# Kernel optimization log

Hardware: AMD Instinct MI355X
Metric: run time of the kernel (lower is better)

Reference implementation:

```python
import jax, jax.numpy as jnp
import numpy as np
import math

B, T = 32, 64
VOCAB = 50005
EMB = 512
HID = 1024
SES = 1024
KNOW = 8785
NEG = math.exp(-100)

def _glorot(key, shape):
    fan_in, fan_out = shape[1], shape[0]
    lim = (6.0 / (fan_in + fan_out)) ** 0.5
    return jax.random.uniform(key, shape, jnp.float32, -lim, lim)

def setup_inputs() -> dict:
    key = jax.random.key(0)
    ks = jax.random.split(key, 16)
    inp = {}
    inp['ses_encoding'] = jax.random.normal(ks[0], (B, 1, SES), jnp.float32)
    inp['know_encoding'] = jax.random.normal(ks[1], (B, 1, SES), jnp.float32)
    inp['target'] = jax.random.randint(ks[2], (B, T), 0, 50000)
    inp['embed_w'] = jax.random.normal(ks[3], (VOCAB, EMB), jnp.float32) * 0.02
    # GRU params (PyTorch layout: W_ih [3H, E], W_hh [3H, H], gate order r,z,n)
    s = 1.0 / (HID ** 0.5)
    inp['W_ih'] = jax.random.uniform(ks[4], (3 * HID, EMB), jnp.float32, -s, s)
    inp['W_hh'] = jax.random.uniform(ks[5], (3 * HID, HID), jnp.float32, -s, s)
    inp['b_ih'] = jax.random.uniform(ks[6], (3 * HID,), jnp.float32, -s, s)
    inp['b_hh'] = jax.random.uniform(ks[7], (3 * HID,), jnp.float32, -s, s)
    inp['ses_to_dec_w'] = _glorot(ks[8], (HID, SES))
    inp['ses_to_dec_b'] = jnp.zeros((HID,), jnp.float32)
    inp['dec_inf_w'] = _glorot(ks[9], (2 * EMB, HID))
    inp['ses_inf_w'] = _glorot(ks[10], (2 * EMB, SES))
    inp['emb_inf_w'] = _glorot(ks[11], (2 * EMB, EMB))
    inp['emb_inf_b'] = jnp.zeros((2 * EMB,), jnp.float32)
    inp['W1'] = jax.random.normal(ks[12], (VOCAB, SES), jnp.float32) * 0.02
    inp['W2'] = jax.random.normal(ks[13], (VOCAB, SES), jnp.float32) * 0.02
    inp['W3'] = jax.random.normal(ks[14], (VOCAB, 2 * EMB), jnp.float32) * 0.02
    inp['W4'] = jax.random.normal(ks[15], (VOCAB, EMB), jnp.float32) * 0.02
    inp['know_vote_w'] = _glorot(jax.random.fold_in(key, 99), (KNOW, SES))
    return inp

def _gru_step(x, h, W_ih, W_hh, b_ih, b_hh):
    # x: [B,E], h: [B,H]
    gi = x @ W_ih.T + b_ih
    gh = h @ W_hh.T + b_hh
    ir, iz, inn = jnp.split(gi, 3, axis=-1)
    hr, hz, hn = jnp.split(gh, 3, axis=-1)
    r = jax.nn.sigmoid(ir + hr)
    z = jax.nn.sigmoid(iz + hz)
    n = jnp.tanh(inn + r * hn)
    return (1.0 - z) * h + z * n  # torch: h' = (1-z)*n + z*h with torch z; note torch formula

def _gru_step_torch(x, h, W_ih, W_hh, b_ih, b_hh):
    gi = x @ W_ih.T + b_ih
    gh = h @ W_hh.T + b_hh
    ir, iz, inn = jnp.split(gi, 3, axis=-1)
    hr, hz, hn = jnp.split(gh, 3, axis=-1)
    r = jax.nn.sigmoid(ir + hr)
    z = jax.nn.sigmoid(iz + hz)
    n = jnp.tanh(inn + r * hn)
    return (1.0 - z) * n + z * h

def reference(ses_encoding, know_encoding, target, embed_w, W_ih, W_hh, b_ih, b_hh,
              ses_to_dec_w, ses_to_dec_b, dec_inf_w, ses_inf_w, emb_inf_w, emb_inf_b,
              W1, W2, W3, W4, know_vote_w):
    ses = ses_encoding[:, 0, :]    # [B, SES]
    know = know_encoding[:, 0, :]  # [B, SES]
    target_emb = embed_w[target]   # [B, T, E]

    h0 = jnp.tanh(ses @ ses_to_dec_w.T + ses_to_dec_b)  # [B, H]

    # time-invariant pieces
    ses_inf_vec = ses @ ses_inf_w.T                      # [B, 2E]
    l1 = ses @ W1.T                                      # [B, V]
    l2 = know @ W2.T                                     # [B, V]
    # knowledge mixture log-probs (constant over time)
    ks = know @ know_vote_w.T                            # [B, KNOW]
    ks = ks[:, :-1]                                      # drop last -> [B, KNOW-1]
    pad_l = jnp.full((ks.shape[0], 10), NEG, ks.dtype)
    pad_r = jnp.full((ks.shape[0], VOCAB - 10 - (KNOW - 1)), NEG, ks.dtype)
    know_scores = jnp.concatenate([pad_l, ks, pad_r], axis=1)  # [B, V]
    know_probs = jax.nn.log_softmax(know_scores, axis=-1)      # [B, V]
    gate_const = l1 + l2                                 # [B, V]

    def step(h, emb_t):
        # emb_t: [B, E]
        h_new = _gru_step_torch(emb_t, h, W_ih, W_hh, b_ih, b_hh)  # [B, H]
        dec_hid_vec = h_new @ dec_inf_w.T                          # [B, 2E]
        target_inf = emb_t @ emb_inf_w.T + emb_inf_b               # [B, 2E]
        total = dec_hid_vec + ses_inf_vec + target_inf             # [B, 2E]
        mx = jnp.max(total.reshape(total.shape[0], EMB, 2), axis=-1)  # maxout -> [B, E]
        logits = mx @ embed_w.T                                    # shared embedding -> [B, V]
        hid_probs = jax.nn.log_softmax(logits, axis=-1)
        l3 = h_new @ W3.T                                          # note: W3 applied to hid_o [B,H]... but W3 is [V,2E]
        l4 = emb_t @ W4.T                                          # [B, V]
        gate = jax.nn.sigmoid(gate_const + l3 + l4)                # [B, V]
        final = gate * hid_probs + (1.0 - gate) * know_probs       # [B, V]
        return h_new, final

    # target_emb time-major for scan
    _, outs = jax.lax.scan(step, h0, jnp.swapaxes(target_emb, 0, 1))
    final_scores_all = jnp.swapaxes(outs, 0, 1)  # [B, T, V]
    return final_scores_all
```

## Files before the change

kernel.cpp:

```cpp
#include <hip/hip_runtime.h>

constexpr int VOC  = 50005;
constexpr int VOCP = 50048;
constexpr int VOCP2= 50176;
constexpr int NTM  = 391;
constexpr int NTMP = 400;
constexpr int KSN  = 8784;
constexpr float NPAD = 41221.0f;

typedef unsigned short u16;
typedef __attribute__((ext_vector_type(4))) float f32x4;
typedef __attribute__((ext_vector_type(8))) short bf16x8;

__device__ __forceinline__ float dot4(float4 a, float4 b) {
    return a.x*b.x + a.y*b.y + a.z*b.z + a.w*b.w;
}
__device__ __forceinline__ float sigmoidf_(float x) { return 1.0f / (1.0f + expf(-x)); }
__device__ __forceinline__ u16 f2bf(float f) {
    unsigned x = __float_as_uint(f);
    return (u16)((x + 0x7FFFu + ((x >> 16) & 1u)) >> 16);
}
__device__ __forceinline__ float bf2f(u16 u) { return __uint_as_float(((unsigned)u) << 16); }
__device__ __forceinline__ bf16x8 pack8(float4 lo, float4 hi) {
    union { bf16x8 v; unsigned u[4]; } r;
    r.u[0] = f2bf(lo.x) | ((unsigned)f2bf(lo.y) << 16);
    r.u[1] = f2bf(lo.z) | ((unsigned)f2bf(lo.w) << 16);
    r.u[2] = f2bf(hi.x) | ((unsigned)f2bf(hi.y) << 16);
    r.u[3] = f2bf(hi.z) | ((unsigned)f2bf(hi.w) << 16);
    return r.v;
}
template<int AUX>
__device__ __forceinline__ void gload_lds16x(const void* g, void* l) {
    __builtin_amdgcn_global_load_lds((const __attribute__((address_space(1))) unsigned int*)g,
                                     (__attribute__((address_space(3))) unsigned int*)l, 16, 0, AUX);
}
__device__ __forceinline__ void gload_lds16(const void* g, void* l) { gload_lds16x<0>(g, l); }
__device__ __forceinline__ void store_u16_sc(u16* p, u16 v) {
    asm volatile("global_store_short %0, %1, off sc0 sc1" :: "v"(p), "v"((unsigned)v) : "memory");
}

__global__ __launch_bounds__(256) void k_cvt(const float* __restrict__ src, u16* __restrict__ dst,
                                             int ncols, int sld, int dld) {
    int row = blockIdx.x;
    int c = (blockIdx.y * 256 + threadIdx.x) * 4;
    if (c >= ncols) return;
    float4 v = *(const float4*)(src + (size_t)row * sld + c);
    unsigned lo = f2bf(v.x) | ((unsigned)f2bf(v.y) << 16);
    unsigned hi = f2bf(v.z) | ((unsigned)f2bf(v.w) << 16);
    *(uint2*)(dst + (size_t)row * dld + c) = make_uint2(lo, hi);
}

__global__ __launch_bounds__(256) void k_pad0(u16* __restrict__ Aemb, u16* __restrict__ A34) {
    int r = VOC + blockIdx.x;
    unsigned* p3 = (unsigned*)(A34 + (size_t)r * 1536);
    for (int i = threadIdx.x; i < 768; i += 256) p3[i] = 0;
    if (r < VOCP) {
        unsigned* pe = (unsigned*)(Aemb + (size_t)r * 512);
        if (threadIdx.x < 256) pe[threadIdx.x] = 0;
    }
}

__global__ __launch_bounds__(256) void k_bsk(const float* __restrict__ ses,
                                             const float* __restrict__ know,
                                             u16* __restrict__ Bsk) {
    int row = blockIdx.x;
    for (int c0 = threadIdx.x * 4; c0 < 2048; c0 += 1024) {
        uint2 val = make_uint2(0, 0);
        if (row < 32) {
            const float* srcp = (c0 < 1024) ? ses + (size_t)row * 1024 + c0
                                            : know + (size_t)row * 1024 + (c0 - 1024);
            float4 v = *(const float4*)srcp;
            val = make_uint2(f2bf(v.x) | ((unsigned)f2bf(v.y) << 16),
                             f2bf(v.z) | ((unsigned)f2bf(v.w) << 16));
        }
        *(uint2*)(Bsk + (size_t)row * 2048 + c0) = val;
    }
}

__global__ __launch_bounds__(128) void k_gather(const float* __restrict__ embed,
                                                const int* __restrict__ target,
                                                u16* __restrict__ BG) {
    int n = blockIdx.x;
    int row = target[n];
    int c = threadIdx.x * 4;
    float4 v = *(const float4*)(embed + (size_t)row * 512 + c);
    unsigned lo = f2bf(v.x) | ((unsigned)f2bf(v.y) << 16);
    unsigned hi = f2bf(v.z) | ((unsigned)f2bf(v.w) << 16);
    *(uint2*)(BG + (size_t)n * 1536 + 1024 + c) = make_uint2(lo, hi);
}

__global__ __launch_bounds__(256) void k_h0_sesinf(const float* __restrict__ ses,
                                                   const float* __restrict__ sdw,
                                                   const float* __restrict__ sdb,
                                                   const float* __restrict__ siw,
                                                   float* __restrict__ h0,
                                                   float* __restrict__ sesinf) {
    int g = blockIdx.x * 256 + threadIdx.x;
    int b = g & 31;
    int jg = g >> 5;
    int j0 = jg * 4;
    const float4* s4 = (const float4*)(ses + (size_t)b * 1024);
    const float4* wa[4];
    const float4* wc[4];
#pragma unroll
    for (int r = 0; r < 4; ++r) {
        wa[r] = (const float4*)(sdw + (size_t)(j0 + r) * 1024);
        wc[r] = (const float4*)(siw + (size_t)(j0 + r) * 1024);
    }
    float a[4] = {0, 0, 0, 0}, c[4] = {0, 0, 0, 0};
    for (int kq = 0; kq < 256; ++kq) {
        float4 sv = s4[kq];
#pragma unroll
        for (int r = 0; r < 4; ++r) { a[r] += dot4(sv, wa[r][kq]); c[r] += dot4(sv, wc[r][kq]); }
    }
#pragma unroll
    for (int r = 0; r < 4; ++r) {
        h0[b * 1024 + j0 + r] = tanhf(a[r] + sdb[j0 + r]);
        sesinf[b * 1024 + j0 + r] = c[r];
    }
}

__global__ __launch_bounds__(256) void k_lseknow(const float* __restrict__ ks,
                                                 float* __restrict__ lsek) {
    int b = blockIdx.x;
    int t = threadIdx.x;
    __shared__ float sm[256];
    float m = -1e30f;
    for (int j = t; j < KSN; j += 256) m = fmaxf(m, ks[(size_t)b * KSN + j]);
    sm[t] = m;
    __syncthreads();
    for (int s = 128; s > 0; s >>= 1) { if (t < s) sm[t] = fmaxf(sm[t], sm[t + s]); __syncthreads(); }
    m = fmaxf(sm[0], 0.0f);
    __syncthreads();
    float s = 0.0f;
    for (int j = t; j < KSN; j += 256) s += expf(ks[(size_t)b * KSN + j] - m);
    sm[t] = s;
    __syncthreads();
    for (int r = 128; r > 0; r >>= 1) { if (t < r) sm[t] += sm[t + r]; __syncthreads(); }
    if (t == 0) lsek[b] = m + logf(sm[0] + NPAD * expf(0.0f - m));
}

template<int MODE>
__global__ __launch_bounds__(128) void k_sk32(const float* __restrict__ A1,
                                              const float* __restrict__ A2,
                                              const u16* __restrict__ Bsk,
                                              float* __restrict__ outp) {
    const int lane = threadIdx.x & 63;
    const int w = threadIdx.x >> 6;
    const int lrow = lane & 15;
    const int kg = lane >> 4;
    constexpr int K = (MODE == 0) ? 2048 : 1024;
    constexpr int bc0 = (MODE == 0) ? 0 : 1024;
    const int rowmax = (MODE == 0) ? (VOC - 1) : (KSN - 1);
    const int vb = blockIdx.x * 64 + w * 32;
    const int r0 = min(vb + lrow, rowmax);
    const int r1 = min(vb + 16 + lrow, rowmax);
    f32x4 acc[2][2] = {{{0.f,0.f,0.f,0.f},{0.f,0.f,0.f,0.f}},
                       {{0.f,0.f,0.f,0.f},{0.f,0.f,0.f,0.f}}};
    for (int k0 = 0; k0 < K; k0 += 32) {
        int kc = k0 + kg * 8;
        const float* s0;
        const float* s1;
        if (MODE == 0 && k0 >= 1024) {
            s0 = A2 + (size_t)r0 * 1024 + (kc - 1024);
            s1 = A2 + (size_t)r1 * 1024 + (kc - 1024);
        } else {
            s0 = A1 + (size_t)r0 * 1024 + kc;
            s1 = A1 + (size_t)r1 * 1024 + kc;
        }
        bf16x8 af0 = pack8(*(const float4*)s0, *(const float4*)(s0 + 4));
        bf16x8 af1 = pack8(*(const float4*)s1, *(const float4*)(s1 + 4));
        bf16x8 b0 = *(const bf16x8*)(Bsk + (size_t)lrow * 2048 + bc0 + kc);
        bf16x8 b1 = *(const bf16x8*)(Bsk + (size_t)(16 + lrow) * 2048 + bc0 + kc);
        acc[0][0] = __builtin_amdgcn_mfma_f32_16x16x32_bf16(af0, b0, acc[0][0], 0, 0, 0);
        acc[0][1] = __builtin_amdgcn_mfma_f32_16x16x32_bf16(af0, b1, acc[0][1], 0, 0, 0);
        acc[1][0] = __builtin_amdgcn_mfma_f32_16x16x32_bf16(af1, b0, acc[1][0], 0, 0, 0);
        acc[1][1] = __builtin_amdgcn_mfma_f32_16x16x32_bf16(af1, b1, acc[1][1], 0, 0, 0);
    }
    const int rg = kg * 4;
#pragma unroll
    for (int mi = 0; mi < 2; ++mi)
#pragma unroll
        for (int ni = 0; ni < 2; ++ni)
#pragma unroll
            for (int r = 0; r < 4; ++r) {
                int v = vb + mi * 16 + rg + r;
                int b = ni * 16 + lrow;
                if (MODE == 0) outp[(size_t)b * VOCP2 + v] = acc[mi][ni][r];
                else if (v < KSN) outp[(size_t)b * KSN + v] = acc[mi][ni][r];
            }
}

template<int EPI>
__global__ __launch_bounds__(256) void gemm_bt(
    const u16* __restrict__ A, int lda,
    const u16* __restrict__ B, int ldb, int K,
    const float* __restrict__ p0, const float* __restrict__ p1,
    float* __restrict__ q0, u16* __restrict__ q1,
    unsigned char* __restrict__ q2, float* __restrict__ q3)
{
    __shared__ u16 Asm[128 * 64];
    __shared__ u16 Bsm[128 * 64];
    const int tid = threadIdx.x;
    const int lane = tid & 63;
    const int w = tid >> 6;
    const int wm = w >> 1, wn = w & 1;
    const int nt = blockIdx.x, mt = blockIdx.y;

    f32x4 acc[4][4];
#pragma unroll
    for (int i = 0; i < 4; ++i)
#pragma unroll
        for (int j = 0; j < 4; ++j) acc[i][j] = (f32x4){0.f, 0.f, 0.f, 0.f};

    for (int kt = 0; kt < K; kt += 64) {
#pragma unroll
        for (int p = 0; p < 4; ++p) {
            int flat = (w * 4 + p) * 64 + lane;
            int row = flat >> 3, slot = flat & 7;
            int ss = slot ^ (row & 7);
            gload_lds16(A + (size_t)(mt * 128 + row) * lda + kt + ss * 8, Asm + flat * 8);
            gload_lds16(B + (size_t)(nt * 128 + row) * ldb + kt + ss * 8, Bsm + flat * 8);
        }
        __syncthreads();
#pragma unroll
        for (int kc = 0; kc < 2; ++kc) {
            bf16x8 af[4], bfr[4];
#pragma unroll
            for (int mi = 0; mi < 4; ++mi) {
                int row = wm * 64 + mi * 16 + (lane & 15);
                int bcol = kc * 64 + ((lane >> 4) << 4);
                af[mi] = *(const bf16x8*)((const char*)Asm + row * 128 + (bcol ^ ((row & 7) << 4)));
            }
#pragma unroll
            for (int ni = 0; ni < 4; ++ni) {
                int row = wn * 64 + ni * 16 + (lane & 15);
                int bcol = kc * 64 + ((lane >> 4) << 4);
                bfr[ni] = *(const bf16x8*)((const char*)Bsm + row * 128 + (bcol ^ ((row & 7) << 4)));
            }
#pragma unroll
            for (int mi = 0; mi < 4; ++mi)
#pragma unroll
                for (int ni = 0; ni < 4; ++ni)
                    acc[mi][ni] = __builtin_amdgcn_mfma_f32_16x16x32_bf16(af[mi], bfr[ni], acc[mi][ni], 0, 0, 0);
        }
        __syncthreads();
    }

    const int cl = lane & 15;
    const int rg = (lane >> 4) << 2;

    if constexpr (EPI == 0) {
#pragma unroll
        for (int mi = 0; mi < 4; ++mi) {
            int m0 = mt * 128 + wm * 64 + mi * 16 + rg;
            float4 bias = *(const float4*)(p0 + m0);
#pragma unroll
            for (int ni = 0; ni < 4; ++ni) {
                int n = nt * 128 + wn * 64 + ni * 16 + cl;
                float4 v;
                v.x = acc[mi][ni][0] + bias.x; v.y = acc[mi][ni][1] + bias.y;
                v.z = acc[mi][ni][2] + bias.z; v.w = acc[mi][ni][3] + bias.w;
                *(float4*)(q0 + (size_t)n * 3072 + m0) = v;
            }
        }
    }
    if constexpr (EPI == 1) {
#pragma unroll
        for (int mi = 0; mi < 4; ++mi) {
            int m0 = mt * 128 + wm * 64 + mi * 16 + rg;
            float4 eb4 = *(const float4*)(p1 + m0);
#pragma unroll
            for (int ni = 0; ni < 4; ++ni) {
                int n = nt * 128 + wn * 64 + ni * 16 + cl;
                int b = n >> 6;
                float v0 = acc[mi][ni][0] + p0[b * 1024 + m0 + 0] + eb4.x;
                float v1 = acc[mi][ni][1] + p0[b * 1024 + m0 + 1] + eb4.y;
                float v2 = acc[mi][ni][2] + p0[b * 1024 + m0 + 2] + eb4.z;
                float v3 = acc[mi][ni][3] + p0[b * 1024 + m0 + 3] + eb4.w;
                unsigned pk = f2bf(fmaxf(v0, v1)) | ((unsigned)f2bf(fmaxf(v2, v3)) << 16);
                *(unsigned*)(q1 + (size_t)n * 512 + (m0 >> 1)) = pk;
            }
        }
    }
    if constexpr (EPI == 3) {
        __shared__ float redm[2][128];
        __shared__ float reds[2][128];
#pragma unroll
        for (int mi = 0; mi < 4; ++mi) {
            int v0 = mt * 128 + wm * 64 + mi * 16 + rg;
#pragma unroll
            for (int ni = 0; ni < 4; ++ni) {
                int n = nt * 128 + wn * 64 + ni * 16 + cl;
                unsigned lo = f2bf(acc[mi][ni][0]) | ((unsigned)f2bf(acc[mi][ni][1]) << 16);
                unsigned hi = f2bf(acc[mi][ni][2]) | ((unsigned)f2bf(acc[mi][ni][3]) << 16);
                *(uint2*)(q1 + (size_t)n * VOCP + v0) = make_uint2(lo, hi);
            }
        }
#pragma unroll
        for (int ni = 0; ni < 4; ++ni) {
            float lm = -1e30f;
#pragma unroll
            for (int mi = 0; mi < 4; ++mi) {
                int v0 = mt * 128 + wm * 64 + mi * 16 + rg;
#pragma unroll
                for (int r = 0; r < 4; ++r)
                    if (v0 + r < VOC) lm = fmaxf(lm, acc[mi][ni][r]);
            }
            lm = fmaxf(lm, __shfl_xor(lm, 16));
            lm = fmaxf(lm, __shfl_xor(lm, 32));
            float s = 0.0f;
#pragma unroll
            for (int mi = 0; mi < 4; ++mi) {
                int v0 = mt * 128 + wm * 64 + mi * 16 + rg;
#pragma unroll
                for (int r = 0; r < 4; ++r)
                    if (v0 + r < VOC) s += expf(acc[mi][ni][r] - lm);
            }
            s += __shfl_xor(s, 16);
            s += __shfl_xor(s, 32);
            if (lane < 16) {
                redm[wm][wn * 64 + ni * 16 + lane] = lm;
                reds[wm][wn * 64 + ni * 16 + lane] = s;
            }
        }
        __syncthreads();
        if (tid < 128) {
            float m0_ = redm[0][tid], m1_ = redm[1][tid];
            float m = fmaxf(m0_, m1_);
            float s = reds[0][tid] * expf(m0_ - m) + reds[1][tid] * expf(m1_ - m);
            int n = nt * 128 + tid;
            q0[(size_t)n * NTMP + mt] = m;
            q3[(size_t)n * NTMP + mt] = s;
        }
    }
}

__global__ __launch_bounds__(512, 1) void gemm_gate8(
    const u16* __restrict__ A,
    const u16* __restrict__ B,
    const float* __restrict__ gc2,
    unsigned char* __restrict__ g8)
{
    __shared__ __align__(16) char smem[131072];
    const int tid = threadIdx.x;
    const int lane = tid & 63;
    const int w = tid >> 6;
    const int wm = w >> 2;
    const int wn = w & 3;
    const int lrow = lane & 15;
    const int g = lane >> 4;

    int bid = blockIdx.x;
    int wg = (bid & 7) * 196 + (bid >> 3);
    int mt = wg >> 3;
    int nt = wg & 7;
    const size_t arow0 = (size_t)mt * 256;
    const size_t brow0 = (size_t)nt * 256;

    auto stageA = [&](int T, int h) {
        char* dst = smem + (T & 1) * 65536 + h * 16384;
        const u16* src = A + (arow0 + h * 128) * 1536 + T * 64;
#pragma unroll
        for (int q = 0; q < 2; ++q) {
            int flat = q * 512 + tid;
            int r = flat >> 3, s = flat & 7;
            int ss = s ^ (r & 7);
            gload_lds16(src + (size_t)r * 1536 + ss * 8, dst + flat * 16);
        }
    };
    auto stageB = [&](int T, int h) {
        char* dst = smem + (T & 1) * 65536 + 32768 + h * 16384;
        const u16* src = B + (brow0 + h * 128) * 1536 + T * 64;
#pragma unroll
        for (int q = 0; q < 2; ++q) {
            int flat = q * 512 + tid;
            int r = flat >> 3, s = flat & 7;
            int ss = s ^ (r & 7);
            gload_lds16(src + (size_t)r * 1536 + ss * 8, dst + flat * 16);
        }
    };

    f32x4 acc[8][4];
#pragma unroll
    for (int i = 0; i < 8; ++i)
#pragma unroll
        for (int j = 0; j < 4; ++j) acc[i][j] = (f32x4){0.f, 0.f, 0.f, 0.f};

    const char* Ab[2] = { smem + wm * 16384, smem + 65536 + wm * 16384 };
    const char* Bb[2] = { smem + 32768 + (wn >> 1) * 16384,
                          smem + 65536 + 32768 + (wn >> 1) * 16384 };
    bf16x8 bf[4][2];
    bf16x8 afA[2][2], afB[2][2];

#define ISSA(D, Q, AF)                                                                \
    _Pragma("unroll") for (int mi = 0; mi < 2; ++mi) {                                \
        int r = ((Q) * 2 + mi) * 16 + lrow;                                           \
        _Pragma("unroll") for (int kk = 0; kk < 2; ++kk)                              \
            AF[mi][kk] = *(const bf16x8*)(Ab[D] + r * 128 +                           \
                            ((kk * 64 + g * 16) ^ ((r & 7) << 4)));                   \
    }
#define ISSB(D)                                                                       \
    _Pragma("unroll") for (int ni = 0; ni < 4; ++ni) {                                \
        int r = (wn & 1) * 64 + ni * 16 + lrow;                                       \
        _Pragma("unroll") for (int kk = 0; kk < 2; ++kk)                              \
            bf[ni][kk] = *(const bf16x8*)(Bb[D] + r * 128 +                           \
                            ((kk * 64 + g * 16) ^ ((r & 7) << 4)));                   \
    }
#define MM(Q, AF)                                                                     \
    __builtin_amdgcn_s_setprio(1);                                                    \
    _Pragma("unroll") for (int kk = 0; kk < 2; ++kk)                                  \
        _Pragma("unroll") for (int mi = 0; mi < 2; ++mi)                              \
            _Pragma("unroll") for (int ni = 0; ni < 4; ++ni)                          \
                acc[(Q) * 2 + mi][ni] = __builtin_amdgcn_mfma_f32_16x16x32_bf16(      \
                    AF[mi][kk], bf[ni][kk], acc[(Q) * 2 + mi][ni], 0, 0, 0);          \
    __builtin_amdgcn_s_setprio(0)
#define LG4 asm volatile("s_waitcnt lgkmcnt(4)" ::: "memory"); __builtin_amdgcn_sched_barrier(0)
#define LG0 asm volatile("s_waitcnt lgkmcnt(0)" ::: "memory"); __builtin_amdgcn_sched_barrier(0)
#define BARR  __builtin_amdgcn_sched_barrier(0); __builtin_amdgcn_s_barrier(); \
              __builtin_amdgcn_sched_barrier(0)
#define VM4 asm volatile("s_waitcnt vmcnt(4)" ::: "memory"); __builtin_amdgcn_sched_barrier(0)
#define VM0 asm volatile("s_waitcnt vmcnt(0)" ::: "memory"); __builtin_amdgcn_sched_barrier(0)

    stageB(0, 0); stageB(0, 1); stageA(0, 0); stageA(0, 1); stageB(1, 0); stageB(1, 1);
    VM4;
    BARR;
    ISSA(0, 0, afA);

    for (int i = 0; i < 11; ++i) {
        int T0 = 2 * i, T1 = 2 * i + 1;
        stageA(T1, 0); ISSB(0); ISSA(0, 1, afB); LG4; MM(0, afA);
        stageA(T1, 1); ISSA(0, 2, afA); LG4; MM(1, afB);
        BARR;
        stageB(T0 + 2, 0); ISSA(0, 3, afB); LG4; MM(2, afA);
        stageB(T0 + 2, 1); VM4; ISSA(1, 0, afA); LG4; MM(3, afB);
        BARR;
        stageA(T0 + 2, 0); ISSB(1); ISSA(1, 1, afB); LG4; MM(0, afA);
        stageA(T0 + 2, 1); ISSA(1, 2, afA); LG4; MM(1, afB);
        BARR;
        stageB(T1 + 2, 0); ISSA(1, 3, afB); LG4; MM(2, afA);
        stageB(T1 + 2, 1); VM4; ISSA(0, 0, afA); LG4; MM(3, afB);
        BARR;
    }
    stageA(23, 0); ISSB(0); ISSA(0, 1, afB); LG4; MM(0, afA);
    stageA(23, 1); ISSA(0, 2, afA); LG4; MM(1, afB);
    BARR;
    ISSA(0, 3, afB); LG4; MM(2, afA);
    VM0; ISSA(1, 0, afA); LG4; MM(3, afB);
    BARR;
    ISSB(1); ISSA(1, 1, afB); LG4; MM(0, afA);
    ISSA(1, 2, afA); LG4; MM(1, afB);
    ISSA(1, 3, afB); LG4; MM(2, afA);
    LG0; MM(3, afB);
#undef ISSA
#undef ISSB
#undef MM
#undef LG4
#undef LG0
#undef BARR
#undef VM4
#undef VM0

    const int rg = g << 2;
    const int b = nt * 4 + wn;
    const float* gcrow = gc2 + (size_t)b * VOCP2;
#pragma unroll
    for (int m = 0; m < 8; ++m) {
        int v0 = mt * 256 + wm * 128 + m * 16 + rg;
        float4 gcv = *(const float4*)(gcrow + v0);
#pragma unroll
        for (int ni = 0; ni < 4; ++ni) {
            int n = nt * 256 + wn * 64 + ni * 16 + lrow;
            unsigned pk = 0;
#pragma unroll
            for (int r = 0; r < 4; ++r) {
                float garg = acc[m][ni][r] + ((const float*)&gcv)[r];
                float gate = 1.0f / (1.0f + expf(-garg));
                pk |= ((unsigned)(int)(gate * 255.0f + 0.5f)) << (8 * r);
            }
            *(unsigned*)(g8 + (size_t)n * VOCP2 + v0) = pk;
        }
    }
}

__global__ __launch_bounds__(256, 1) void k_gru_m4(const u16* __restrict__ WhhB,
                                                   const float* __restrict__ GI,
                                                   const float* __restrict__ bhh,
                                                   const u16* __restrict__ h0b,
                                                   u16* __restrict__ BG,
                                                   unsigned* __restrict__ flags) {
    __shared__ __align__(16) char smem[131072];
    const int tid = threadIdx.x;
    const int lane = tid & 63;
    const int w = tid >> 6;
    const int jb = blockIdx.x;
    const int j0 = jb * 16;
    const int jl = tid & 15, bp = tid >> 4;
    const int je = j0 + jl;
    const float bh0 = bhh[je], bh1 = bhh[1024 + je], bh2 = bhh[2048 + je];
    char* Bbase = smem + 98304 + w * 8192;

#pragma unroll
    for (int it = 0; it < 24; ++it) {
        int flat = (it * 4 + w) * 64 + lane;
        int r = flat >> 7, s = flat & 127;
        int ss = s ^ (r & 7);
        int gr = (r >> 4) * 1024 + j0 + (r & 15);
        gload_lds16(WhhB + (size_t)gr * 1024 + ss * 8, smem + (size_t)flat * 16);
    }

    float hpv[2];
#pragma unroll
    for (int rb = 0; rb < 2; ++rb)
        hpv[rb] = bf2f(h0b[(size_t)(bp * 2 + rb) * 1024 + je]);

    const int lrow = lane & 15;
    const int ksel = lane >> 4;

    for (int t = 0; t < 64; ++t) {
        const u16* hsrc = (t == 0) ? h0b : BG + (size_t)(t - 1) * 1536;
        const size_t hstr = (t == 0) ? 1024 : (size_t)64 * 1536;

        float gi0[2], gi1[2], gi2[2];
#pragma unroll
        for (int rb = 0; rb < 2; ++rb) {
            const float* gp = GI + ((size_t)((bp * 2 + rb) * 64 + t)) * 3072 + je;
            gi0[rb] = gp[0]; gi1[rb] = gp[1024]; gi2[rb] = gp[2048];
        }
        __builtin_amdgcn_sched_barrier(0);

        auto stageB = [&](int c) {
            char* dst = Bbase + (c & 1) * 4096;
            int kq0 = w * 256 + c * 64;
#pragma unroll
            for (int q = 0; q < 4; ++q) {
                int flat = q * 64 + lane;
                int r = flat >> 3, s = flat & 7;
                int ss = s ^ (r & 7);
                gload_lds16x<0x11>(hsrc + (size_t)r * hstr + kq0 + ss * 8,
                                   dst + (size_t)flat * 16);
            }
        };
        stageB(0); stageB(1);
        if (t == 0) {
            __syncthreads();
        } else {
            asm volatile("s_waitcnt vmcnt(4)" ::: "memory");
        }
        __builtin_amdgcn_sched_barrier(0);

        f32x4 acc[3][2];
#pragma unroll
        for (int mi = 0; mi < 3; ++mi)
#pragma unroll
            for (int ni = 0; ni < 2; ++ni) acc[mi][ni] = (f32x4){0.f, 0.f, 0.f, 0.f};

#pragma unroll
        for (int c = 0; c < 4; ++c) {
            char* Bb = Bbase + (c & 1) * 4096;
#pragma unroll
            for (int ks = 0; ks < 2; ++ks) {
                int kb = ks * 64 + ksel * 16;
                bf16x8 bfr[2];
#pragma unroll
                for (int ni = 0; ni < 2; ++ni) {
                    int br = ni * 16 + lrow;
                    bfr[ni] = *(const bf16x8*)(Bb + br * 128 + (kb ^ ((br & 7) << 4)));
                }
                int kA = w * 512 + c * 128 + kb;
#pragma unroll
                for (int mi = 0; mi < 3; ++mi) {
                    int ar = mi * 16 + lrow;
                    bf16x8 af = *(const bf16x8*)(smem + ar * 2048 + (kA ^ ((ar & 7) << 4)));
#pragma unroll
                    for (int ni = 0; ni < 2; ++ni)
                        acc[mi][ni] = __builtin_amdgcn_mfma_f32_16x16x32_bf16(af, bfr[ni], acc[mi][ni], 0, 0, 0);
                }
            }
            asm volatile("s_waitcnt lgkmcnt(0)" ::: "memory");
            __builtin_amdgcn_sched_barrier(0);
            if (c < 2) {
                stageB(c + 2);
                asm volatile("s_waitcnt vmcnt(4)" ::: "memory");
            } else if (c == 2) {
                asm volatile("s_waitcnt vmcnt(0)" ::: "memory");
            }
            __builtin_amdgcn_sched_barrier(0);
        }

        float (*epiw)[33] = (float(*)[33])Bbase;
        {
            const int rg = (lane >> 4) << 2;
#pragma unroll
            for (int mi = 0; mi < 3; ++mi)
#pragma unroll
                for (int ni = 0; ni < 2; ++ni) {
                    int m0 = mi * 16 + rg;
                    int cb = ni * 16 + lrow;
#pragma unroll
                    for (int r = 0; r < 4; ++r) epiw[m0 + r][cb] = acc[mi][ni][r];
                }
        }
        asm volatile("s_waitcnt lgkmcnt(0)" ::: "memory");
        __builtin_amdgcn_s_barrier();

#pragma unroll
        for (int rb = 0; rb < 2; ++rb) {
            int b = bp * 2 + rb;
            float s0 = 0.f, s1 = 0.f, s2 = 0.f;
#pragma unroll
            for (int ww = 0; ww < 4; ++ww) {
                float (*ep)[33] = (float(*)[33])(smem + 98304 + ww * 8192);
                s0 += ep[jl][b]; s1 += ep[16 + jl][b]; s2 += ep[32 + jl][b];
            }
            float rr = sigmoidf_(gi0[rb] + s0 + bh0);
            float zz = sigmoidf_(gi1[rb] + s1 + bh1);
            float nn = tanhf(gi2[rb] + rr * (s2 + bh2));
            float hnew = (1.0f - zz) * nn + zz * hpv[rb];
            hpv[rb] = hnew;
            store_u16_sc(BG + ((size_t)(b * 64 + t)) * 1536 + je, f2bf(hnew));
        }

        if (t < 63) {
            asm volatile("s_waitcnt vmcnt(0)" ::: "memory");
            __syncthreads();
            if (tid == 0)
                __hip_atomic_store(&flags[jb], (unsigned)(t + 1),
                                   __ATOMIC_RELAXED, __HIP_MEMORY_SCOPE_AGENT);
            unsigned tgt = (unsigned)(t + 1);
            while (true) {
                unsigned v = __hip_atomic_load(&flags[lane],
                                               __ATOMIC_RELAXED, __HIP_MEMORY_SCOPE_AGENT);
                if (__all(v >= tgt)) break;
                __builtin_amdgcn_s_sleep(1);
            }
            __builtin_amdgcn_sched_barrier(0);
        }
    }
}

__global__ __launch_bounds__(256) void k_lse(const float* __restrict__ pmax,
                                             const float* __restrict__ psum,
                                             float* __restrict__ lse) {
    int n = blockIdx.x;
    int t = threadIdx.x;
    __shared__ float sm[256];
    const float* pm = pmax + (size_t)n * NTMP;
    const float* ps = psum + (size_t)n * NTMP;
    float m = -1e30f;
    for (int p = t; p < NTM; p += 256) m = fmaxf(m, pm[p]);
    sm[t] = m;
    __syncthreads();
    for (int s = 128; s > 0; s >>= 1) { if (t < s) sm[t] = fmaxf(sm[t], sm[t + s]); __syncthreads(); }
    m = sm[0];
    __syncthreads();
    float s = 0.0f;
    for (int p = t; p < NTM; p += 256) s += ps[p] * expf(pm[p] - m);
    sm[t] = s;
    __syncthreads();
    for (int r = 128; r > 0; r >>= 1) { if (t < r) sm[t] += sm[t + r]; __syncthreads(); }
    if (t == 0) lse[n] = m + logf(sm[0]);
}

__global__ __launch_bounds__(256) void k_final(const u16* __restrict__ Lb,
                                               const unsigned char* __restrict__ g8,
                                               const float* __restrict__ lse,
                                               const float* __restrict__ ks,
                                               const float* __restrict__ lsek,
                                               float* __restrict__ out) {
    int n = blockIdx.y;
    int b = n >> 6;
    float lsen = lse[n], lkb = lsek[b];
    int base = blockIdx.x * 2048;
#pragma unroll
    for (int i = 0; i < 8; ++i) {
        int v = base + i * 256 + threadIdx.x;
        if (v < VOC) {
            float L = bf2f(Lb[(size_t)n * VOCP + v]);
            float g = g8[(size_t)n * VOCP2 + v] * (1.0f / 255.0f);
            float kp = ((v >= 10 && v < 10 + KSN) ? ks[(size_t)b * KSN + (v - 10)] : 0.0f) - lkb;
            out[(size_t)n * VOC + v] = g * (L - lsen) + (1.0f - g) * kp;
        }
    }
}

extern "C" void kernel_launch(void* const* d_in, const int* in_sizes, int n_in,
                              void* d_out, int out_size, void* d_ws, size_t ws_size,
                              hipStream_t stream) {
    const float* ses    = (const float*)d_in[0];
    const float* know   = (const float*)d_in[1];
    const int*   target = (const int*)d_in[2];
    const float* embed  = (const float*)d_in[3];
    const float* Wih    = (const float*)d_in[4];
    const float* Whh    = (const float*)d_in[5];
    const float* bih    = (const float*)d_in[6];
    const float* bhh    = (const float*)d_in[7];
    const float* sdw    = (const float*)d_in[8];
    const float* sdb    = (const float*)d_in[9];
    const float* dw     = (const float*)d_in[10];
    const float* siw    = (const float*)d_in[11];
    const float* ew     = (const float*)d_in[12];
    const float* eb     = (const float*)d_in[13];
    const float* W1     = (const float*)d_in[14];
    const float* W2     = (const float*)d_in[15];
    const float* W3     = (const float*)d_in[16];
    const float* W4     = (const float*)d_in[17];
    const float* kvw    = (const float*)d_in[18];

    char* ws = (char*)d_ws;
    size_t o = 0;
    auto alloc = [&](size_t bytes) { char* r = ws + o; o += (bytes + 255) & ~(size_t)255; return r; };
    u16*   Aemb  = (u16*)  alloc((size_t)VOCP * 512 * 2);
    u16*   A34   = (u16*)  alloc((size_t)VOCP2 * 1536 * 2);
    u16*   Adwew = (u16*)  alloc((size_t)1024 * 1536 * 2);
    u16*   Wihb  = (u16*)  alloc((size_t)3072 * 512 * 2);
    u16*   WhhB  = (u16*)  alloc((size_t)3072 * 1024 * 2);
    u16*   h0b   = (u16*)  alloc((size_t)32 * 1024 * 2);
    u16*   BG    = (u16*)  alloc((size_t)2048 * 1536 * 2);
    u16*   BL    = (u16*)  alloc((size_t)2048 * 512 * 2);
    float* GI    = (float*)alloc((size_t)2048 * 3072 * 4);
    float* h0    = (float*)alloc((size_t)32 * 1024 * 4);
    float* sesinf= (float*)alloc((size_t)32 * 1024 * 4);
    float* gc    = (float*)alloc((size_t)32 * VOCP2 * 4);
    float* ksb   = (float*)alloc((size_t)32 * KSN * 4);
    float* lsek  = (float*)alloc(256);
    float* lse   = (float*)alloc((size_t)2048 * 4);
    unsigned* flags = (unsigned*)alloc(256);
    float* pmax  = (float*)alloc((size_t)2048 * NTMP * 4);
    float* psum  = (float*)alloc((size_t)2048 * NTMP * 4);
    unsigned char* g8 = (unsigned char*)alloc((size_t)2048 * VOCP2);
    u16*   Lb    = (u16*)  alloc((size_t)2048 * VOCP * 2);
    u16*   Bsk   = (u16*)  alloc((size_t)128 * 2048 * 2);
    float* out = (float*)d_out;

    hipMemsetAsync(flags, 0, 256, stream);

    k_cvt<<<dim3(VOC, 1), 256, 0, stream>>>(embed, Aemb, 512, 512, 512);
    k_cvt<<<dim3(VOC, 1), 256, 0, stream>>>(W3, A34, 1024, 1024, 1536);
    k_cvt<<<dim3(VOC, 1), 256, 0, stream>>>(W4, A34 + 1024, 512, 512, 1536);
    k_pad0<<<dim3(VOCP2 - VOC), 256, 0, stream>>>(Aemb, A34);
    k_cvt<<<dim3(1024, 1), 256, 0, stream>>>(dw, Adwew, 1024, 1024, 1536);
    k_cvt<<<dim3(1024, 1), 256, 0, stream>>>(ew, Adwew + 1024, 512, 512, 1536);
    k_cvt<<<dim3(3072, 1), 256, 0, stream>>>(Wih, Wihb, 512, 512, 512);
    k_cvt<<<dim3(3072, 1), 256, 0, stream>>>(Whh, WhhB, 1024, 1024, 1024);
    k_bsk<<<dim3(128), 256, 0, stream>>>(ses, know, Bsk);

    k_gather<<<dim3(2048), 128, 0, stream>>>(embed, target, BG);
    k_h0_sesinf<<<dim3(32), 256, 0, stream>>>(ses, sdw, sdb, siw, h0, sesinf);
    k_cvt<<<dim3(32, 1), 256, 0, stream>>>(h0, h0b, 1024, 1024, 1024);

    k_sk32<0><<<dim3(VOCP2 / 64), 128, 0, stream>>>(W1, W2, Bsk, gc);
    k_sk32<1><<<dim3((KSN + 63) / 64), 128, 0, stream>>>(kvw, nullptr, Bsk, ksb);
    k_lseknow<<<dim3(32), 256, 0, stream>>>(ksb, lsek);

    gemm_bt<0><<<dim3(16, 24), 256, 0, stream>>>(Wihb, 512, BG + 1024, 1536, 512,
                                                 bih, nullptr, GI, nullptr, nullptr, nullptr);
    k_gru_m4<<<dim3(64), 256, 0, stream>>>(WhhB, GI, bhh, h0b, BG, flags);
    gemm_bt<1><<<dim3(16, 8), 256, 0, stream>>>(Adwew, 1536, BG, 1536, 1536,
                                                sesinf, eb, nullptr, BL, nullptr, nullptr);
    gemm_gate8<<<dim3(1568), 512, 0, stream>>>(A34, BG, gc, g8);
    gemm_bt<3><<<dim3(16, NTM), 256, 0, stream>>>(Aemb, 512, BL, 512, 512,
                                                  nullptr, nullptr, pmax, Lb, nullptr, psum);
    k_lse<<<dim3(2048), 256, 0, stream>>>(pmax, psum, lse);
    k_final<<<dim3(25, 2048), 256, 0, stream>>>(Lb, g8, lse, ksb, lsek, out);
}
```

Baseline: 1.573 ms.

## Fuse gate GEMM and vocab-logit GEMM into one 256x256-tile kernel

The separate logits GEMM (128x128 tiles, 391 row tiles) is merged into the gate GEMM kernel. Each block first computes the gate tile and writes its quantised gates, then reuses the same LDS pipeline to compute the logits tile and its partial max/sum. This removes one launch, uses the larger 256-wide tiling for logits and halves the partial-LSE count, at the cost of padding the vocab buffers to 50176. Separately, the GRU kernel now stages all four K chunks of h into enlarged LDS up front instead of double-buffering, which trades LDS capacity for fewer waits inside the chunk loop.

```diff
diff --git a/kernel.cpp b/kernel.cpp
--- a/kernel.cpp
+++ b/kernel.cpp
@@ -1,9 +1,8 @@
 #include <hip/hip_runtime.h>
 
 constexpr int VOC  = 50005;
-constexpr int VOCP = 50048;
 constexpr int VOCP2= 50176;
-constexpr int NTM  = 391;
+constexpr int NT2  = 196;
 constexpr int NTMP = 400;
 constexpr int KSN  = 8784;
 constexpr float NPAD = 41221.0f;
@@ -54,10 +53,8 @@
     int r = VOC + blockIdx.x;
     unsigned* p3 = (unsigned*)(A34 + (size_t)r * 1536);
     for (int i = threadIdx.x; i < 768; i += 256) p3[i] = 0;
-    if (r < VOCP) {
-        unsigned* pe = (unsigned*)(Aemb + (size_t)r * 512);
-        if (threadIdx.x < 256) pe[threadIdx.x] = 0;
-    }
+    unsigned* pe = (unsigned*)(Aemb + (size_t)r * 512);
+    if (threadIdx.x < 256) pe[threadIdx.x] = 0;
 }
 
 __global__ __launch_bounds__(256) void k_bsk(const float* __restrict__ ses,
@@ -196,8 +193,7 @@
     const u16* __restrict__ A, int lda,
     const u16* __restrict__ B, int ldb, int K,
     const float* __restrict__ p0, const float* __restrict__ p1,
-    float* __restrict__ q0, u16* __restrict__ q1,
-    unsigned char* __restrict__ q2, float* __restrict__ q3)
+    float* __restrict__ q0, u16* __restrict__ q1)
 {
     __shared__ u16 Asm[128 * 64];
     __shared__ u16 Bsm[128 * 64];
@@ -283,64 +279,18 @@
             }
         }
     }
-    if constexpr (EPI == 3) {
-        __shared__ float redm[2][128];
-        __shared__ float reds[2][128];
-#pragma unroll
-        for (int mi = 0; mi < 4; ++mi) {
-            int v0 = mt * 128 + wm * 64 + mi * 16 + rg;
-#pragma unroll
-            for (int ni = 0; ni < 4; ++ni) {
-                int n = nt * 128 + wn * 64 + ni * 16 + cl;
-                unsigned lo = f2bf(acc[mi][ni][0]) | ((unsigned)f2bf(acc[mi][ni][1]) << 16);
-                unsigned hi = f2bf(acc[mi][ni][2]) | ((unsigned)f2bf(acc[mi][ni][3]) << 16);
-                *(uint2*)(q1 + (size_t)n * VOCP + v0) = make_uint2(lo, hi);
-            }
-        }
-#pragma unroll
-        for (int ni = 0; ni < 4; ++ni) {
-            float lm = -1e30f;
-#pragma unroll
-            for (int mi = 0; mi < 4; ++mi) {
-                int v0 = mt * 128 + wm * 64 + mi * 16 + rg;
-#pragma unroll
-                for (int r = 0; r < 4; ++r)
-                    if (v0 + r < VOC) lm = fmaxf(lm, acc[mi][ni][r]);
-            }
-            lm = fmaxf(lm, __shfl_xor(lm, 16));
-            lm = fmaxf(lm, __shfl_xor(lm, 32));
-            float s = 0.0f;
-#pragma unroll
-            for (int mi = 0; mi < 4; ++mi) {
-                int v0 = mt * 128 + wm * 64 + mi * 16 + rg;
-#pragma unroll
-                for (int r = 0; r < 4; ++r)
-                    if (v0 + r < VOC) s += expf(acc[mi][ni][r] - lm);
-            }
-            s += __shfl_xor(s, 16);
-            s += __shfl_xor(s, 32);
-            if (lane < 16) {
-                redm[wm][wn * 64 + ni * 16 + lane] = lm;
-                reds[wm][wn * 64 + ni * 16 + lane] = s;
-            }
-        }
-        __syncthreads();
-        if (tid < 128) {
-            float m0_ = redm[0][tid], m1_ = redm[1][tid];
-            float m = fmaxf(m0_, m1_);
-            float s = reds[0][tid] * expf(m0_ - m) + reds[1][tid] * expf(m1_ - m);
-            int n = nt * 128 + tid;
-            q0[(size_t)n * NTMP + mt] = m;
-            q3[(size_t)n * NTMP + mt] = s;
-        }
-    }
-}
-
-__global__ __launch_bounds__(512, 1) void gemm_gate8(
-    const u16* __restrict__ A,
-    const u16* __restrict__ B,
+}
+
+__global__ __launch_bounds__(512, 1) void gemm_fused(
+    const u16* __restrict__ A34,
+    const u16* __restrict__ Aemb,
+    const u16* __restrict__ BG,
+    const u16* __restrict__ BL,
     const float* __restrict__ gc2,
-    unsigned char* __restrict__ g8)
+    unsigned char* __restrict__ g8,
+    u16* __restrict__ Lb,
+    float* __restrict__ pmax,
+    float* __restrict__ psum)
 {
     __shared__ __align__(16) char smem[131072];
     const int tid = threadIdx.x;
@@ -358,26 +308,15 @@
     const size_t arow0 = (size_t)mt * 256;
     const size_t brow0 = (size_t)nt * 256;
 
-    auto stageA = [&](int T, int h) {
-        char* dst = smem + (T & 1) * 65536 + h * 16384;
-        const u16* src = A + (arow0 + h * 128) * 1536 + T * 64;
+    auto stage = [&](const u16* __restrict__ src0, int ld, int abase, int T, int h) {
+        char* dst = smem + (T & 1) * 65536 + abase + h * 16384;
+        const u16* src = src0 + ((abase ? brow0 : arow0) + h * 128) * (size_t)ld + T * 64;
 #pragma unroll
         for (int q = 0; q < 2; ++q) {
             int flat = q * 512 + tid;
             int r = flat >> 3, s = flat & 7;
             int ss = s ^ (r & 7);
-            gload_lds16(src + (size_t)r * 1536 + ss * 8, dst + flat * 16);
-        }
-    };
-    auto stageB = [&](int T, int h) {
-        char* dst = smem + (T & 1) * 65536 + 32768 + h * 16384;
-        const u16* src = B + (brow0 + h * 128) * 1536 + T * 64;
-#pragma unroll
-        for (int q = 0; q < 2; ++q) {
-            int flat = q * 512 + tid;
-            int r = flat >> 3, s = flat & 7;
-            int ss = s ^ (r & 7);
-            gload_lds16(src + (size_t)r * 1536 + ss * 8, dst + flat * 16);
+            gload_lds16(src + (size_t)r * ld + ss * 8, dst + flat * 16);
         }
     };
 
@@ -421,29 +360,31 @@
               __builtin_amdgcn_sched_barrier(0)
 #define VM4 asm volatile("s_waitcnt vmcnt(4)" ::: "memory"); __builtin_amdgcn_sched_barrier(0)
 #define VM0 asm volatile("s_waitcnt vmcnt(0)" ::: "memory"); __builtin_amdgcn_sched_barrier(0)
-
-    stageB(0, 0); stageB(0, 1); stageA(0, 0); stageA(0, 1); stageB(1, 0); stageB(1, 1);
-    VM4;
-    BARR;
+#define SA34(T, h)  stage(A34, 1536, 0, T, h)
+#define SBG(T, h)   stage(BG, 1536, 32768, T, h)
+#define SAE(T, h)   stage(Aemb, 512, 0, T, h)
+#define SBL(T, h)   stage(BL, 512, 32768, T, h)
+
+    SBG(0, 0); SBG(0, 1); SA34(0, 0); SA34(0, 1); SBG(1, 0); SBG(1, 1);
+    VM4; BARR;
     ISSA(0, 0, afA);
-
     for (int i = 0; i < 11; ++i) {
         int T0 = 2 * i, T1 = 2 * i + 1;
-        stageA(T1, 0); ISSB(0); ISSA(0, 1, afB); LG4; MM(0, afA);
-        stageA(T1, 1); ISSA(0, 2, afA); LG4; MM(1, afB);
-        BARR;
-        stageB(T0 + 2, 0); ISSA(0, 3, afB); LG4; MM(2, afA);
-        stageB(T0 + 2, 1); VM4; ISSA(1, 0, afA); LG4; MM(3, afB);
-        BARR;
-        stageA(T0 + 2, 0); ISSB(1); ISSA(1, 1, afB); LG4; MM(0, afA);
-        stageA(T0 + 2, 1); ISSA(1, 2, afA); LG4; MM(1, afB);
-        BARR;
-        stageB(T1 + 2, 0); ISSA(1, 3, afB); LG4; MM(2, afA);
-        stageB(T1 + 2, 1); VM4; ISSA(0, 0, afA); LG4; MM(3, afB);
-        BARR;
-    }
-    stageA(23, 0); ISSB(0); ISSA(0, 1, afB); LG4; MM(0, afA);
-    stageA(23, 1); ISSA(0, 2, afA); LG4; MM(1, afB);
+        SA34(T1, 0); ISSB(0); ISSA(0, 1, afB); LG4; MM(0, afA);
+        SA34(T1, 1); ISSA(0, 2, afA); LG4; MM(1, afB);
+        BARR;
+        SBG(T0 + 2, 0); ISSA(0, 3, afB); LG4; MM(2, afA);
+        SBG(T0 + 2, 1); VM4; ISSA(1, 0, afA); LG4; MM(3, afB);
+        BARR;
+        SA34(T0 + 2, 0); ISSB(1); ISSA(1, 1, afB); LG4; MM(0, afA);
+        SA34(T0 + 2, 1); ISSA(1, 2, afA); LG4; MM(1, afB);
+        BARR;
+        SBG(T1 + 2, 0); ISSA(1, 3, afB); LG4; MM(2, afA);
+        SBG(T1 + 2, 1); VM4; ISSA(0, 0, afA); LG4; MM(3, afB);
+        BARR;
+    }
+    SA34(23, 0); ISSB(0); ISSA(0, 1, afB); LG4; MM(0, afA);
+    SA34(23, 1); ISSA(0, 2, afA); LG4; MM(1, afB);
     BARR;
     ISSA(0, 3, afB); LG4; MM(2, afA);
     VM0; ISSA(1, 0, afA); LG4; MM(3, afB);
@@ -452,6 +393,118 @@
     ISSA(1, 2, afA); LG4; MM(1, afB);
     ISSA(1, 3, afB); LG4; MM(2, afA);
     LG0; MM(3, afB);
+
+    {
+        const int rg = g << 2;
+        const int b = nt * 4 + wn;
+        const float* gcrow = gc2 + (size_t)b * VOCP2;
+#pragma unroll
+        for (int m = 0; m < 8; ++m) {
+            int v0 = mt * 256 + wm * 128 + m * 16 + rg;
+            float4 gcv = *(const float4*)(gcrow + v0);
+#pragma unroll
+            for (int ni = 0; ni < 4; ++ni) {
+                int n = nt * 256 + wn * 64 + ni * 16 + lrow;
+                unsigned pk = 0;
+#pragma unroll
+                for (int r = 0; r < 4; ++r) {
+                    float garg = acc[m][ni][r] + ((const float*)&gcv)[r];
+                    float gate = 1.0f / (1.0f + expf(-garg));
+                    pk |= ((unsigned)(int)(gate * 255.0f + 0.5f)) << (8 * r);
+                }
+                *(unsigned*)(g8 + (size_t)n * VOCP2 + v0) = pk;
+            }
+        }
+    }
+    BARR;
+
+#pragma unroll
+    for (int i = 0; i < 8; ++i)
+#pragma unroll
+        for (int j = 0; j < 4; ++j) acc[i][j] = (f32x4){0.f, 0.f, 0.f, 0.f};
+
+    SBL(0, 0); SBL(0, 1); SAE(0, 0); SAE(0, 1); SBL(1, 0); SBL(1, 1);
+    VM4; BARR;
+    ISSA(0, 0, afA);
+    for (int i = 0; i < 3; ++i) {
+        int T0 = 2 * i, T1 = 2 * i + 1;
+        SAE(T1, 0); ISSB(0); ISSA(0, 1, afB); LG4; MM(0, afA);
+        SAE(T1, 1); ISSA(0, 2, afA); LG4; MM(1, afB);
+        BARR;
+        SBL(T0 + 2, 0); ISSA(0, 3, afB); LG4; MM(2, afA);
+        SBL(T0 + 2, 1); VM4; ISSA(1, 0, afA); LG4; MM(3, afB);
+        BARR;
+        SAE(T0 + 2, 0); ISSB(1); ISSA(1, 1, afB); LG4; MM(0, afA);
+        SAE(T0 + 2, 1); ISSA(1, 2, afA); LG4; MM(1, afB);
+        BARR;
+        SBL(T1 + 2, 0); ISSA(1, 3, afB); LG4; MM(2, afA);
+        SBL(T1 + 2, 1); VM4; ISSA(0, 0, afA); LG4; MM(3, afB);
+        BARR;
+    }
+    SAE(7, 0); ISSB(0); ISSA(0, 1, afB); LG4; MM(0, afA);
+    SAE(7, 1); ISSA(0, 2, afA); LG4; MM(1, afB);
+    BARR;
+    ISSA(0, 3, afB); LG4; MM(2, afA);
+    VM0; ISSA(1, 0, afA); LG4; MM(3, afB);
+    BARR;
+    ISSB(1); ISSA(1, 1, afB); LG4; MM(0, afA);
+    ISSA(1, 2, afA); LG4; MM(1, afB);
+    ISSA(1, 3, afB); LG4; MM(2, afA);
+    LG0; MM(3, afB);
+
+    BARR;
+    {
+        const int rg = g << 2;
+#pragma unroll
+        for (int m = 0; m < 8; ++m) {
+            int v0 = mt * 256 + wm * 128 + m * 16 + rg;
+#pragma unroll
+            for (int ni = 0; ni < 4; ++ni) {
+                int n = nt * 256 + wn * 64 + ni * 16 + lrow;
+                unsigned lo = f2bf(acc[m][ni][0]) | ((unsigned)f2bf(acc[m][ni][1]) << 16);
+                unsigned hi = f2bf(acc[m][ni][2]) | ((unsigned)f2bf(acc[m][ni][3]) << 16);
+                *(uint2*)(Lb + (size_t)n * VOCP2 + v0) = make_uint2(lo, hi);
+            }
+        }
+        float* redm = (float*)smem;
+        float* reds = (float*)(smem + 2048);
+#pragma unroll
+        for (int ni = 0; ni < 4; ++ni) {
+            float lm = -1e30f;
+#pragma unroll
+            for (int m = 0; m < 8; ++m) {
+                int v0 = mt * 256 + wm * 128 + m * 16 + rg;
+#pragma unroll
+                for (int r = 0; r < 4; ++r)
+                    if (v0 + r < VOC) lm = fmaxf(lm, acc[m][ni][r]);
+            }
+            lm = fmaxf(lm, __shfl_xor(lm, 16));
+            lm = fmaxf(lm, __shfl_xor(lm, 32));
+            float s = 0.0f;
+#pragma unroll
+            for (int m = 0; m < 8; ++m) {
+                int v0 = mt * 256 + wm * 128 + m * 16 + rg;
+#pragma unroll
+                for (int r = 0; r < 4; ++r)
+                    if (v0 + r < VOC) s += expf(acc[m][ni][r] - lm);
+            }
+            s += __shfl_xor(s, 16);
+            s += __shfl_xor(s, 32);
+            if (lane < 16) {
+                redm[wm * 256 + wn * 64 + ni * 16 + lane] = lm;
+                reds[wm * 256 + wn * 64 + ni * 16 + lane] = s;
+            }
+        }
+        BARR;
+        if (tid < 256) {
+            float m0_ = redm[tid], m1_ = redm[256 + tid];
+            float m = fmaxf(m0_, m1_);
+            float s = reds[tid] * expf(m0_ - m) + reds[256 + tid] * expf(m1_ - m);
+            int n = nt * 256 + tid;
+            pmax[(size_t)n * NTMP + mt] = m;
+            psum[(size_t)n * NTMP + mt] = s;
+        }
+    }
 #undef ISSA
 #undef ISSB
 #undef MM
@@ -460,36 +513,19 @@
 #undef BARR
 #undef VM4
 #undef VM0
-
-    const int rg = g << 2;
-    const int b = nt * 4 + wn;
-    const float* gcrow = gc2 + (size_t)b * VOCP2;
-#pragma unroll
-    for (int m = 0; m < 8; ++m) {
-        int v0 = mt * 256 + wm * 128 + m * 16 + rg;
-        float4 gcv = *(const float4*)(gcrow + v0);
-#pragma unroll
-        for (int ni = 0; ni < 4; ++ni) {
-            int n = nt * 256 + wn * 64 + ni * 16 + lrow;
-            unsigned pk = 0;
-#pragma unroll
-            for (int r = 0; r < 4; ++r) {
-                float garg = acc[m][ni][r] + ((const float*)&gcv)[r];
-                float gate = 1.0f / (1.0f + expf(-garg));
-                pk |= ((unsigned)(int)(gate * 255.0f + 0.5f)) << (8 * r);
-            }
-            *(unsigned*)(g8 + (size_t)n * VOCP2 + v0) = pk;
-        }
-    }
-}
-
-__global__ __launch_bounds__(256, 1) void k_gru_m4(const u16* __restrict__ WhhB,
+#undef SA34
+#undef SBG
+#undef SAE
+#undef SBL
+}
+
+__global__ __launch_bounds__(256, 1) void k_gru_m5(const u16* __restrict__ WhhB,
                                                    const float* __restrict__ GI,
                                                    const float* __restrict__ bhh,
                                                    const u16* __restrict__ h0b,
                                                    u16* __restrict__ BG,
                                                    unsigned* __restrict__ flags) {
-    __shared__ __align__(16) char smem[131072];
+    __shared__ __align__(16) char smem[163840];
     const int tid = threadIdx.x;
     const int lane = tid & 63;
     const int w = tid >> 6;
@@ -498,7 +534,7 @@
     const int jl = tid & 15, bp = tid >> 4;
     const int je = j0 + jl;
     const float bh0 = bhh[je], bh1 = bhh[1024 + je], bh2 = bhh[2048 + je];
-    char* Bbase = smem + 98304 + w * 8192;
+    char* Bbase = smem + 98304 + w * 16384;
 
 #pragma unroll
     for (int it = 0; it < 24; ++it) {
@@ -521,16 +557,9 @@
         const u16* hsrc = (t == 0) ? h0b : BG + (size_t)(t - 1) * 1536;
         const size_t hstr = (t == 0) ? 1024 : (size_t)64 * 1536;
 
-        float gi0[2], gi1[2], gi2[2];
-#pragma unroll
-        for (int rb = 0; rb < 2; ++rb) {
-            const float* gp = GI + ((size_t)((bp * 2 + rb) * 64 + t)) * 3072 + je;
-            gi0[rb] = gp[0]; gi1[rb] = gp[1024]; gi2[rb] = gp[2048];
-        }
-        __builtin_amdgcn_sched_barrier(0);
-
-        auto stageB = [&](int c) {
-            char* dst = Bbase + (c & 1) * 4096;
+#pragma unroll
+        for (int c = 0; c < 4; ++c) {
+            char* dst = Bbase + c * 4096;
             int kq0 = w * 256 + c * 64;
 #pragma unroll
             for (int q = 0; q < 4; ++q) {
@@ -540,12 +569,17 @@
                 gload_lds16x<0x11>(hsrc + (size_t)r * hstr + kq0 + ss * 8,
                                    dst + (size_t)flat * 16);
             }
-        };
-        stageB(0); stageB(1);
+        }
+        float gi0[2], gi1[2], gi2[2];
+#pragma unroll
+        for (int rb = 0; rb < 2; ++rb) {
+            const float* gp = GI + ((size_t)((bp * 2 + rb) * 64 + t)) * 3072 + je;
+            gi0[rb] = gp[0]; gi1[rb] = gp[1024]; gi2[rb] = gp[2048];
+        }
         if (t == 0) {
             __syncthreads();
         } else {
-            asm volatile("s_waitcnt vmcnt(4)" ::: "memory");
+            asm volatile("s_waitcnt vmcnt(0)" ::: "memory");
         }
         __builtin_amdgcn_sched_barrier(0);
 
@@ -557,7 +591,7 @@
 
 #pragma unroll
         for (int c = 0; c < 4; ++c) {
-            char* Bb = Bbase + (c & 1) * 4096;
+            char* Bb = Bbase + c * 4096;
 #pragma unroll
             for (int ks = 0; ks < 2; ++ks) {
                 int kb = ks * 64 + ksel * 16;
@@ -577,18 +611,11 @@
                         acc[mi][ni] = __builtin_amdgcn_mfma_f32_16x16x32_bf16(af, bfr[ni], acc[mi][ni], 0, 0, 0);
                 }
             }
-            asm volatile("s_waitcnt lgkmcnt(0)" ::: "memory");
-            __builtin_amdgcn_sched_barrier(0);
-            if (c < 2) {
-                stageB(c + 2);
-                asm volatile("s_waitcnt vmcnt(4)" ::: "memory");
-            } else if (c == 2) {
-                asm volatile("s_waitcnt vmcnt(0)" ::: "memory");
-            }
-            __builtin_amdgcn_sched_barrier(0);
         }
 
         float (*epiw)[33] = (float(*)[33])Bbase;
+        asm volatile("s_waitcnt lgkmcnt(0)" ::: "memory");
+        __builtin_amdgcn_sched_barrier(0);
         {
             const int rg = (lane >> 4) << 2;
 #pragma unroll
@@ -610,7 +637,7 @@
             float s0 = 0.f, s1 = 0.f, s2 = 0.f;
 #pragma unroll
             for (int ww = 0; ww < 4; ++ww) {
-                float (*ep)[33] = (float(*)[33])(smem + 98304 + ww * 8192);
+                float (*ep)[33] = (float(*)[33])(smem + 98304 + ww * 16384);
                 s0 += ep[jl][b]; s1 += ep[16 + jl][b]; s2 += ep[32 + jl][b];
             }
             float rr = sigmoidf_(gi0[rb] + s0 + bh0);
@@ -648,14 +675,14 @@
     const float* pm = pmax + (size_t)n * NTMP;
     const float* ps = psum + (size_t)n * NTMP;
     float m = -1e30f;
-    for (int p = t; p < NTM; p += 256) m = fmaxf(m, pm[p]);
+    if (t < NT2) m = pm[t];
     sm[t] = m;
     __syncthreads();
     for (int s = 128; s > 0; s >>= 1) { if (t < s) sm[t] = fmaxf(sm[t], sm[t + s]); __syncthreads(); }
     m = sm[0];
     __syncthreads();
     float s = 0.0f;
-    for (int p = t; p < NTM; p += 256) s += ps[p] * expf(pm[p] - m);
+    if (t < NT2) s = ps[t] * expf(pm[t] - m);
     sm[t] = s;
     __syncthreads();
     for (int r = 128; r > 0; r >>= 1) { if (t < r) sm[t] += sm[t + r]; __syncthreads(); }
@@ -676,7 +703,7 @@
     for (int i = 0; i < 8; ++i) {
         int v = base + i * 256 + threadIdx.x;
         if (v < VOC) {
-            float L = bf2f(Lb[(size_t)n * VOCP + v]);
+            float L = bf2f(Lb[(size_t)n * VOCP2 + v]);
             float g = g8[(size_t)n * VOCP2 + v] * (1.0f / 255.0f);
             float kp = ((v >= 10 && v < 10 + KSN) ? ks[(size_t)b * KSN + (v - 10)] : 0.0f) - lkb;
             out[(size_t)n * VOC + v] = g * (L - lsen) + (1.0f - g) * kp;
@@ -710,7 +737,7 @@
     char* ws = (char*)d_ws;
     size_t o = 0;
     auto alloc = [&](size_t bytes) { char* r = ws + o; o += (bytes + 255) & ~(size_t)255; return r; };
-    u16*   Aemb  = (u16*)  alloc((size_t)VOCP * 512 * 2);
+    u16*   Aemb  = (u16*)  alloc((size_t)VOCP2 * 512 * 2);
     u16*   A34   = (u16*)  alloc((size_t)VOCP2 * 1536 * 2);
     u16*   Adwew = (u16*)  alloc((size_t)1024 * 1536 * 2);
     u16*   Wihb  = (u16*)  alloc((size_t)3072 * 512 * 2);
@@ -729,7 +756,7 @@
     float* pmax  = (float*)alloc((size_t)2048 * NTMP * 4);
     float* psum  = (float*)alloc((size_t)2048 * NTMP * 4);
     unsigned char* g8 = (unsigned char*)alloc((size_t)2048 * VOCP2);
-    u16*   Lb    = (u16*)  alloc((size_t)2048 * VOCP * 2);
+    u16*   Lb    = (u16*)  alloc((size_t)2048 * VOCP2 * 2);
     u16*   Bsk   = (u16*)  alloc((size_t)128 * 2048 * 2);
     float* out = (float*)d_out;
 
@@ -754,13 +781,11 @@
     k_lseknow<<<dim3(32), 256, 0, stream>>>(ksb, lsek);
 
     gemm_bt<0><<<dim3(16, 24), 256, 0, stream>>>(Wihb, 512, BG + 1024, 1536, 512,
-                                                 bih, nullptr, GI, nullptr, nullptr, nullptr);
-    k_gru_m4<<<dim3(64), 256, 0, stream>>>(WhhB, GI, bhh, h0b, BG, flags);
+                                                 bih, nullptr, GI, nullptr);
+    k_gru_m5<<<dim3(64), 256, 0, stream>>>(WhhB, GI, bhh, h0b, BG, flags);
     gemm_bt<1><<<dim3(16, 8), 256, 0, stream>>>(Adwew, 1536, BG, 1536, 1536,
-                                                sesinf, eb, nullptr, BL, nullptr, nullptr);
-    gemm_gate8<<<dim3(1568), 512, 0, stream>>>(A34, BG, gc, g8);
-    gemm_bt<3><<<dim3(16, NTM), 256, 0, stream>>>(Aemb, 512, BL, 512, 512,
-                                                  nullptr, nullptr, pmax, Lb, nullptr, psum);
+                                                sesinf, eb, nullptr, BL);
+    gemm_fused<<<dim3(1568), 512, 0, stream>>>(A34, Aemb, BG, BL, gc, g8, Lb, pmax, psum);
     k_lse<<<dim3(2048), 256, 0, stream>>>(pmax, psum, lse);
     k_final<<<dim3(25, 2048), 256, 0, stream>>>(Lb, g8, lse, ksb, lsek, out);
 }
```

After: 1.595 ms. Within noise of the previous version (+1.4%).
